# Kernel tuning notes

Hardware: AMD Instinct MI355X
Metric: run time of the kernel (lower is better)

## Reference

```python
import jax, jax.numpy as jnp
import numpy as np

B, KB, SEQ, HID = 8, 16, 512, 768  # batch, two_times_batch, max_length, hidden
NEG_INF = float('-inf')


def _l2_normalize(x, eps=1e-12):
    # torch F.normalize: x / max(||x||_2, eps)
    n = jnp.sqrt(jnp.sum(x * x, axis=-1, keepdims=True))
    return x / jnp.maximum(n, eps)


def setup_inputs() -> dict:
    key = jax.random.key(0)
    k1, k2, k3, k4 = jax.random.split(key, 4)
    return {
        'query_embs': jax.random.normal(k1, (B, SEQ, HID), dtype=jnp.float32),
        'key_embs': jax.random.normal(k2, (KB, SEQ, HID), dtype=jnp.float32),
        'alpha_raw': jnp.float32(0.1),  # learnable scalar, cfg.model.alpha init
        'q_mask': jax.random.randint(k3, (B, SEQ), 0, 2, dtype=jnp.int32),
        'k_mask': jax.random.randint(k4, (KB, SEQ), 0, 2, dtype=jnp.int32),
    }


def reference(query_embs, key_embs, alpha_raw, q_mask, k_mask):
    # cfg: distance_weightning='exp', use_softmax=True, gumbel_temp=None
    qn = _l2_normalize(query_embs)          # [B, S, H]
    kn = _l2_normalize(key_embs)            # [KB, T, H]

    # cosine similarity: [B, KB, S, T]
    sim = jnp.einsum('ish,jth->ijst', qn, kn)

    # exp distance weighting, alpha = leaky_relu(alpha_raw)
    alpha = jax.nn.leaky_relu(alpha_raw)
    pos = jnp.arange(SEQ, dtype=jnp.float32)
    distance = jnp.abs(pos[:, None] - pos[None, :])        # [S, T]
    sim = sim * jnp.exp(-alpha * distance)

    valid = (q_mask[:, None, :, None] != 0) & (k_mask[None, :, None, :] != 0)
    logits = jnp.where(valid, sim, NEG_INF)

    p = jax.nn.softmax(logits, axis=-1)                    # [B, KB, S, T]
    p = jnp.nan_to_num(p, nan=0.0)

    # aggregate normalized keys under attention, dot with queries
    aggregated = jnp.einsum('ijst,jth->ijsh', p, kn)       # [B, KB, S, H]
    scores = jnp.einsum('ish,ijsh->ijs', qn, aggregated)   # [B, KB, S]
    scores = scores * q_mask[:, None, :].astype(scores.dtype)
    return scores.sum(axis=-1)                             # [B, KB]
```

## Files before the change

### kernel.cpp

```cpp
#include <hip/hip_runtime.h>
#include <stdint.h>

#define B_   8
#define KB_  16
#define SEQ_ 512
#define HID_ 768

#define NKB  (HID_ / 32)
#define QRB  (B_  * SEQ_ / 16)
#define KRB  (KB_ * SEQ_ / 16)

typedef __attribute__((ext_vector_type(4))) _Float16 half4;
typedef __attribute__((ext_vector_type(8))) _Float16 half8;
typedef __attribute__((ext_vector_type(4))) float    floatx4;

#define GLOBAL_AS __attribute__((address_space(1)))
#define LDS_AS    __attribute__((address_space(3)))

static __device__ __forceinline__ void async_tile16(const _Float16* g, _Float16* l)
{
    __builtin_amdgcn_global_load_lds((const GLOBAL_AS uint32_t*)g,
                                     (LDS_AS uint32_t*)l, 16, 0, 0);
}

#define LP 776

__global__ __launch_bounds__(256)
void prep_tile(const float* __restrict__ Q, const float* __restrict__ K,
               _Float16* __restrict__ Qt, _Float16* __restrict__ Kt)
{
    const int rb = blockIdx.x;
    const float* src;
    _Float16*    dst;
    if (rb < QRB) { src = Q + (size_t)rb * 16 * HID_;          dst = Qt + (size_t)rb * NKB * 512; }
    else          { src = K + (size_t)(rb - QRB) * 16 * HID_;  dst = Kt + (size_t)(rb - QRB) * NKB * 512; }

    __shared__ _Float16 Ls[16 * LP];
    const int wave = threadIdx.x >> 6;
    const int lane = threadIdx.x & 63;

#pragma unroll
    for (int rr = 0; rr < 4; ++rr) {
        int row = wave * 4 + rr;
        const float* s = src + (size_t)row * HID_;
        float4 v[3];
        float ss = 0.f;
#pragma unroll
        for (int it = 0; it < 3; ++it) {
            v[it] = *(const float4*)(s + lane * 4 + it * 256);
            ss += v[it].x * v[it].x + v[it].y * v[it].y + v[it].z * v[it].z + v[it].w * v[it].w;
        }
#pragma unroll
        for (int m = 1; m < 64; m <<= 1) ss += __shfl_xor(ss, m, 64);
        float sc = 1.0f / fmaxf(sqrtf(ss), 1e-12f);
#pragma unroll
        for (int it = 0; it < 3; ++it) {
            half4 h = { (_Float16)(v[it].x * sc), (_Float16)(v[it].y * sc),
                        (_Float16)(v[it].z * sc), (_Float16)(v[it].w * sc) };
            *(half4*)(Ls + row * LP + lane * 4 + it * 256) = h;
        }
    }
    __syncthreads();

#pragma unroll
    for (int rep = 0; rep < 6; ++rep) {
        int slot = rep * 256 + threadIdx.x;
        int kb   = slot >> 6;
        int ln   = slot & 63;
        int row  = ln & 15;
        int ko   = kb * 32 + (ln >> 4) * 8;
        half8 h = *(const half8*)(Ls + row * LP + ko);
        *(half8*)(dst + (size_t)kb * 512 + (size_t)ln * 8) = h;
    }
}

__global__ __launch_bounds__(512, 4)
void li_part(const _Float16* __restrict__ Qt, const _Float16* __restrict__ Kt,
             const float* __restrict__ alpha_p, const int* __restrict__ kmask,
             float* __restrict__ Pbuf)
{
    const int st = blockIdx.x >> 1;
    const int tb = blockIdx.x & 1;
    const int j  = blockIdx.y;
    const int i  = blockIdx.z;

    const int tid  = threadIdx.x;
    const int lane = tid & 63;
    const int wave = tid >> 6;
    const int quad = lane >> 4;
    const int l16  = lane & 15;
    const int wr   = wave >> 2;
    const int wc   = wave & 3;

    __shared__ _Float16 Sbuf[2][24 * 512];
    __shared__ float lred[4][128], nred[4][128];

    const float araw  = *alpha_p;
    const float alpha = araw >= 0.f ? araw : 0.01f * araw;

    const int qbase = i * 32 + st * 8;
    const int kbase = j * 32 + tb * 16;

    const _Float16* gsrc[3];
    _Float16*       ldst0[3];
#pragma unroll
    for (int q = 0; q < 3; ++q) {
        int t   = wave * 3 + q;
        int rbg = (t < 8) ? (qbase + t) : (kbase + (t - 8));
        const _Float16* base = (t < 8) ? Qt : Kt;
        gsrc[q]  = base + (size_t)rbg * NKB * 512 + (size_t)lane * 8;
        ldst0[q] = &Sbuf[0][t * 512];
    }

    floatx4 acc[4][4];
#pragma unroll
    for (int rt = 0; rt < 4; ++rt)
#pragma unroll
        for (int ct = 0; ct < 4; ++ct)
            acc[rt][ct] = (floatx4){0.f, 0.f, 0.f, 0.f};

#pragma unroll
    for (int q = 0; q < 3; ++q)
        async_tile16(gsrc[q], ldst0[q]);

    for (int kb = 0; kb < NKB; ++kb) {
        const int b = kb & 1;
        __syncthreads();
        if (kb + 1 < NKB) {
#pragma unroll
            for (int q = 0; q < 3; ++q)
                async_tile16(gsrc[q] + (size_t)(kb + 1) * 512, ldst0[q] + (b ^ 1) * 24 * 512);
        }
        const _Float16* Qs = &Sbuf[b][0];
        const _Float16* Ks = &Sbuf[b][8 * 512];
        half8 af[4], bf[4];
#pragma unroll
        for (int rt = 0; rt < 4; ++rt)
            af[rt] = *(const half8*)(Qs + (wr * 4 + rt) * 512 + lane * 8);
#pragma unroll
        for (int ct = 0; ct < 4; ++ct)
            bf[ct] = *(const half8*)(Ks + (wc * 4 + ct) * 512 + lane * 8);
#pragma unroll
        for (int rt = 0; rt < 4; ++rt)
#pragma unroll
            for (int ct = 0; ct < 4; ++ct)
                acc[rt][ct] = __builtin_amdgcn_mfma_f32_16x16x32_f16(af[rt], bf[ct], acc[rt][ct], 0, 0, 0);
    }

    const int* km = kmask + j * SEQ_ + tb * 256;
    int kmv[4]; float tgf[4];
#pragma unroll
    for (int ct = 0; ct < 4; ++ct) {
        int t_loc = wc * 64 + ct * 16 + l16;
        kmv[ct] = km[t_loc];
        tgf[ct] = (float)(tb * 256 + t_loc);
    }
#pragma unroll
    for (int rt = 0; rt < 4; ++rt) {
#pragma unroll
        for (int r = 0; r < 4; ++r) {
            float sgf = (float)(st * 128 + wr * 64 + rt * 16 + quad * 4 + r);
            float ps = 0.f, ns = 0.f;
#pragma unroll
            for (int ct = 0; ct < 4; ++ct) {
                float cv = acc[rt][ct][r];
                float e  = kmv[ct] ? __expf(cv * __expf(-alpha * fabsf(sgf - tgf[ct]))) : 0.f;
                ps += e;
                ns += e * cv;
            }
#pragma unroll
            for (int msk = 1; msk < 16; msk <<= 1) {
                ps += __shfl_xor(ps, msk, 64);
                ns += __shfl_xor(ns, msk, 64);
            }
            if (l16 == 0) {
                int rloc = wr * 64 + rt * 16 + quad * 4 + r;
                lred[wc][rloc] = ps;
                nred[wc][rloc] = ns;
            }
        }
    }
    __syncthreads();

    if (tid < 128) {
        float l = lred[0][tid] + lred[1][tid] + lred[2][tid] + lred[3][tid];
        float n = nred[0][tid] + nred[1][tid] + nred[2][tid] + nred[3][tid];
        size_t base = (((size_t)(i * KB_ + j) * SEQ_) + st * 128 + tid) * 4 + tb * 2;
        Pbuf[base]     = l;
        Pbuf[base + 1] = n;
    }
}

__global__ __launch_bounds__(256)
void li_reduce(const float* __restrict__ Pbuf, const int* __restrict__ qmask,
               float* __restrict__ out)
{
    const int ij = blockIdx.x;
    const int i  = ij >> 4;
    const int tid = threadIdx.x;
    __shared__ float red[4];

    float sum = 0.f;
#pragma unroll
    for (int rep = 0; rep < 2; ++rep) {
        int s = tid + rep * 256;
        float4 a = *(const float4*)(Pbuf + ((size_t)ij * SEQ_ + s) * 4);
        float l = a.x + a.z;
        float n = a.y + a.w;
        float sc = (l > 0.f) ? n / l : 0.f;
        if (qmask[i * SEQ_ + s] == 0) sc = 0.f;
        sum += sc;
    }
#pragma unroll
    for (int m = 1; m < 64; m <<= 1) sum += __shfl_xor(sum, m, 64);
    if ((tid & 63) == 0) red[tid >> 6] = sum;
    __syncthreads();
    if (tid == 0) out[ij] = red[0] + red[1] + red[2] + red[3];
}

extern "C" void kernel_launch(void* const* d_in, const int* in_sizes, int n_in,
                              void* d_out, int out_size, void* d_ws, size_t ws_size,
                              hipStream_t stream)
{
    const float* Q       = (const float*)d_in[0];
    const float* K       = (const float*)d_in[1];
    const float* alpha_p = (const float*)d_in[2];
    const int*   qmask   = (const int*)d_in[3];
    const int*   kmask   = (const int*)d_in[4];
    float*       out     = (float*)d_out;

    char* ws = (char*)d_ws;
    _Float16* Qt   = (_Float16*)ws;
    _Float16* Kt   = (_Float16*)(ws + (size_t)B_ * SEQ_ * HID_ * 2);
    float*    Pbuf = (float*)   (ws + (size_t)(B_ + KB_) * SEQ_ * HID_ * 2);

    prep_tile<<<QRB + KRB, 256, 0, stream>>>(Q, K, Qt, Kt);

    dim3 grid(8, KB_, B_);
    li_part<<<grid, 512, 0, stream>>>(Qt, Kt, alpha_p, kmask, Pbuf);

    li_reduce<<<B_ * KB_, 256, 0, stream>>>(Pbuf, qmask, out);
}
```

Baseline: 146.8 us.

## Replace far-distance similarity tiles with a masked key-sum dot product

```diff
diff --git a/kernel.cpp b/kernel.cpp
--- a/kernel.cpp
+++ b/kernel.cpp
@@ -17,6 +17,11 @@
 #define GLOBAL_AS __attribute__((address_space(1)))
 #define LDS_AS    __attribute__((address_space(3)))
 
+#define SKIP_OK(alpha) ((alpha) * 193.f >= 18.f)
+
+#define WS_BASE  ((size_t)(B_ + KB_) * SEQ_ * HID_ * 2 + (size_t)B_ * KB_ * SEQ_ * 4 * sizeof(float))
+#define WS_KTILE ((size_t)KB_ * 32 * 768 * sizeof(float))
+
 static __device__ __forceinline__ void async_tile16(const _Float16* g, _Float16* l)
 {
     __builtin_amdgcn_global_load_lds((const GLOBAL_AS uint32_t*)g,
@@ -27,17 +32,29 @@
 
 __global__ __launch_bounds__(256)
 void prep_tile(const float* __restrict__ Q, const float* __restrict__ K,
-               _Float16* __restrict__ Qt, _Float16* __restrict__ Kt)
+               const int* __restrict__ kmask,
+               _Float16* __restrict__ Qt, _Float16* __restrict__ Kt,
+               float* __restrict__ ktile, int elide)
 {
     const int rb = blockIdx.x;
+    const bool isK = (rb >= QRB);
     const float* src;
     _Float16*    dst;
-    if (rb < QRB) { src = Q + (size_t)rb * 16 * HID_;          dst = Qt + (size_t)rb * NKB * 512; }
-    else          { src = K + (size_t)(rb - QRB) * 16 * HID_;  dst = Kt + (size_t)(rb - QRB) * NKB * 512; }
+    if (!isK) { src = Q + (size_t)rb * 16 * HID_;          dst = Qt + (size_t)rb * NKB * 512; }
+    else      { src = K + (size_t)(rb - QRB) * 16 * HID_;  dst = Kt + (size_t)(rb - QRB) * NKB * 512; }
+    const int rbk  = rb - QRB;
+    const int jj   = rbk >> 5;
+    const int tb16 = rbk & 31;
 
     __shared__ _Float16 Ls[16 * LP];
+    __shared__ float Kred[4 * 768];
     const int wave = threadIdx.x >> 6;
     const int lane = threadIdx.x & 63;
+    const bool doK = isK && (elide != 0);
+
+    float4 ka[3];
+#pragma unroll
+    for (int it = 0; it < 3; ++it) ka[it] = (float4){0.f, 0.f, 0.f, 0.f};
 
 #pragma unroll
     for (int rr = 0; rr < 4; ++rr) {
@@ -58,7 +75,19 @@
             half4 h = { (_Float16)(v[it].x * sc), (_Float16)(v[it].y * sc),
                         (_Float16)(v[it].z * sc), (_Float16)(v[it].w * sc) };
             *(half4*)(Ls + row * LP + lane * 4 + it * 256) = h;
-        }
+            if (doK) {
+                int kmv = kmask[jj * SEQ_ + tb16 * 16 + row];
+                if (kmv) {
+                    ka[it].x += (float)h.x; ka[it].y += (float)h.y;
+                    ka[it].z += (float)h.z; ka[it].w += (float)h.w;
+                }
+            }
+        }
+    }
+    if (doK) {
+#pragma unroll
+        for (int it = 0; it < 3; ++it)
+            *(float4*)(Kred + wave * 768 + lane * 4 + it * 256) = ka[it];
     }
     __syncthreads();
 
@@ -72,12 +101,23 @@
         half8 h = *(const half8*)(Ls + row * LP + ko);
         *(half8*)(dst + (size_t)kb * 512 + (size_t)ln * 8) = h;
     }
+
+    if (doK && threadIdx.x < 192) {
+        int h = threadIdx.x * 4;
+        float4 s0 = *(const float4*)(Kred + h);
+        float4 s1 = *(const float4*)(Kred + 768 + h);
+        float4 s2 = *(const float4*)(Kred + 1536 + h);
+        float4 s3 = *(const float4*)(Kred + 2304 + h);
+        float4 r = { s0.x + s1.x + s2.x + s3.x, s0.y + s1.y + s2.y + s3.y,
+                     s0.z + s1.z + s2.z + s3.z, s0.w + s1.w + s2.w + s3.w };
+        *(float4*)(ktile + ((size_t)jj * 32 + tb16) * 768 + h) = r;
+    }
 }
 
 __global__ __launch_bounds__(512, 4)
 void li_part(const _Float16* __restrict__ Qt, const _Float16* __restrict__ Kt,
              const float* __restrict__ alpha_p, const int* __restrict__ kmask,
-             float* __restrict__ Pbuf)
+             float* __restrict__ Pbuf, int elide)
 {
     const int st = blockIdx.x >> 1;
     const int tb = blockIdx.x & 1;
@@ -97,12 +137,19 @@
 
     const float araw  = *alpha_p;
     const float alpha = araw >= 0.f ? araw : 0.01f * araw;
+    const bool skip_en = (elide != 0) && SKIP_OK(alpha);
+
+    const int sB = st * 2 + wr;
+    const int tB = tb * 4 + wc;
+    const int dB = sB - tB;
+    const bool wskip = skip_en && (dB >= 4 || dB <= -4);
 
     const int qbase = i * 32 + st * 8;
     const int kbase = j * 32 + tb * 16;
 
     const _Float16* gsrc[3];
     _Float16*       ldst0[3];
+    bool            need[3];
 #pragma unroll
     for (int q = 0; q < 3; ++q) {
         int t   = wave * 3 + q;
@@ -110,6 +157,13 @@
         const _Float16* base = (t < 8) ? Qt : Kt;
         gsrc[q]  = base + (size_t)rbg * NKB * 512 + (size_t)lane * 8;
         ldst0[q] = &Sbuf[0][t * 512];
+        if (t < 8) need[q] = true;
+        else {
+            int tBq = tb * 4 + ((t - 8) >> 2);
+            int d0 = st * 2 - tBq, d1 = st * 2 + 1 - tBq;
+            bool near = (d0 <= 3 && d0 >= -3) || (d1 <= 3 && d1 >= -3);
+            need[q] = !skip_en || near;
+        }
     }
 
     floatx4 acc[4][4];
@@ -121,7 +175,7 @@
 
 #pragma unroll
     for (int q = 0; q < 3; ++q)
-        async_tile16(gsrc[q], ldst0[q]);
+        if (need[q]) async_tile16(gsrc[q], ldst0[q]);
 
     for (int kb = 0; kb < NKB; ++kb) {
         const int b = kb & 1;
@@ -129,22 +183,24 @@
         if (kb + 1 < NKB) {
 #pragma unroll
             for (int q = 0; q < 3; ++q)
-                async_tile16(gsrc[q] + (size_t)(kb + 1) * 512, ldst0[q] + (b ^ 1) * 24 * 512);
-        }
-        const _Float16* Qs = &Sbuf[b][0];
-        const _Float16* Ks = &Sbuf[b][8 * 512];
-        half8 af[4], bf[4];
-#pragma unroll
-        for (int rt = 0; rt < 4; ++rt)
-            af[rt] = *(const half8*)(Qs + (wr * 4 + rt) * 512 + lane * 8);
-#pragma unroll
-        for (int ct = 0; ct < 4; ++ct)
-            bf[ct] = *(const half8*)(Ks + (wc * 4 + ct) * 512 + lane * 8);
-#pragma unroll
-        for (int rt = 0; rt < 4; ++rt)
+                if (need[q]) async_tile16(gsrc[q] + (size_t)(kb + 1) * 512, ldst0[q] + (b ^ 1) * 24 * 512);
+        }
+        if (!wskip) {
+            const _Float16* Qs = &Sbuf[b][0];
+            const _Float16* Ks = &Sbuf[b][8 * 512];
+            half8 af[4], bf[4];
+#pragma unroll
+            for (int rt = 0; rt < 4; ++rt)
+                af[rt] = *(const half8*)(Qs + (wr * 4 + rt) * 512 + lane * 8);
 #pragma unroll
             for (int ct = 0; ct < 4; ++ct)
-                acc[rt][ct] = __builtin_amdgcn_mfma_f32_16x16x32_f16(af[rt], bf[ct], acc[rt][ct], 0, 0, 0);
+                bf[ct] = *(const half8*)(Ks + (wc * 4 + ct) * 512 + lane * 8);
+#pragma unroll
+            for (int rt = 0; rt < 4; ++rt)
+#pragma unroll
+                for (int ct = 0; ct < 4; ++ct)
+                    acc[rt][ct] = __builtin_amdgcn_mfma_f32_16x16x32_f16(af[rt], bf[ct], acc[rt][ct], 0, 0, 0);
+        }
     }
 
     const int* km = kmask + j * SEQ_ + tb * 256;
@@ -193,12 +249,57 @@
 
 __global__ __launch_bounds__(256)
 void li_reduce(const float* __restrict__ Pbuf, const int* __restrict__ qmask,
-               float* __restrict__ out)
+               const _Float16* __restrict__ Qt, const float* __restrict__ ktile,
+               const float* __restrict__ alpha_p, float* __restrict__ out, int elide)
 {
     const int ij = blockIdx.x;
     const int i  = ij >> 4;
-    const int tid = threadIdx.x;
+    const int j  = ij & 15;
+    const int tid  = threadIdx.x;
+    const int lane = tid & 63;
+    const int wave = tid >> 6;
+
+    __shared__ float wv[768];
+    __shared__ float nfar[512];
     __shared__ float red[4];
+
+    const float araw  = *alpha_p;
+    const float alpha = araw >= 0.f ? araw : 0.01f * araw;
+    const bool skip_en = (elide != 0) && SKIP_OK(alpha);
+
+    if (skip_en) {
+        const int h0 = tid * 3;
+        const float* kt = ktile + (size_t)j * 32 * 768;
+        for (int sB = 0; sB < 8; ++sB) {
+            float a0 = 0.f, a1 = 0.f, a2 = 0.f;
+            for (int t16 = 0; t16 < 32; ++t16) {
+                int d = (t16 >> 2) - sB;
+                if (d >= 4 || d <= -4) {
+                    const float* p = kt + t16 * 768 + h0;
+                    a0 += p[0]; a1 += p[1]; a2 += p[2];
+                }
+            }
+            wv[h0] = a0; wv[h0 + 1] = a1; wv[h0 + 2] = a2;
+            __syncthreads();
+            const _Float16* qb = Qt + ((size_t)i * 32 + sB * 4 + wave) * (NKB * 512)
+                                    + (size_t)lane * 8;
+            const int kq = (lane >> 4) * 8;
+            float p = 0.f;
+            for (int kb = 0; kb < NKB; ++kb) {
+                half8 q8 = *(const half8*)(qb + kb * 512);
+                const float* w8 = wv + kb * 32 + kq;
+#pragma unroll
+                for (int m = 0; m < 8; ++m) p += (float)q8[m] * w8[m];
+            }
+            p += __shfl_xor(p, 16, 64);
+            p += __shfl_xor(p, 32, 64);
+            if (lane < 16) nfar[sB * 64 + wave * 16 + lane] = p;
+            __syncthreads();
+        }
+    } else {
+        nfar[tid] = 0.f; nfar[tid + 256] = 0.f;
+        __syncthreads();
+    }
 
     float sum = 0.f;
 #pragma unroll
@@ -206,7 +307,7 @@
         int s = tid + rep * 256;
         float4 a = *(const float4*)(Pbuf + ((size_t)ij * SEQ_ + s) * 4);
         float l = a.x + a.z;
-        float n = a.y + a.w;
+        float n = a.y + a.w + nfar[s];
         float sc = (l > 0.f) ? n / l : 0.f;
         if (qmask[i * SEQ_ + s] == 0) sc = 0.f;
         sum += sc;
@@ -230,14 +331,17 @@
     float*       out     = (float*)d_out;
 
     char* ws = (char*)d_ws;
-    _Float16* Qt   = (_Float16*)ws;
-    _Float16* Kt   = (_Float16*)(ws + (size_t)B_ * SEQ_ * HID_ * 2);
-    float*    Pbuf = (float*)   (ws + (size_t)(B_ + KB_) * SEQ_ * HID_ * 2);
-
-    prep_tile<<<QRB + KRB, 256, 0, stream>>>(Q, K, Qt, Kt);
+    _Float16* Qt    = (_Float16*)ws;
+    _Float16* Kt    = (_Float16*)(ws + (size_t)B_ * SEQ_ * HID_ * 2);
+    float*    Pbuf  = (float*)   (ws + (size_t)(B_ + KB_) * SEQ_ * HID_ * 2);
+    float*    ktile = (float*)   (ws + WS_BASE);
+
+    const int elide = (ws_size >= WS_BASE + WS_KTILE) ? 1 : 0;
+
+    prep_tile<<<QRB + KRB, 256, 0, stream>>>(Q, K, kmask, Qt, Kt, ktile, elide);
 
     dim3 grid(8, KB_, B_);
-    li_part<<<grid, 512, 0, stream>>>(Qt, Kt, alpha_p, kmask, Pbuf);
-
-    li_reduce<<<B_ * KB_, 256, 0, stream>>>(Pbuf, qmask, out);
-}
+    li_part<<<grid, 512, 0, stream>>>(Qt, Kt, alpha_p, kmask, Pbuf, elide);
+
+    li_reduce<<<B_ * KB_, 256, 0, stream>>>(Pbuf, qmask, Qt, ktile, alpha_p, out, elide);
+}
```

New measurement: 211.9 us. +44.3%, slower.
